# Optimization experiments

Measured on AMD Instinct MI355X. Metric: run time of the kernel, lower is better.

The kernel has to match this reference:

```python
import jax, jax.numpy as jnp
import numpy as np

N_NODES = 10000   # n_entity
VOCAB = 50000     # nvoc
EMBED = 300       # nembed
HID = 256         # nhid
REP = 8           # words per node name


def setup_inputs() -> dict:
    key = jax.random.key(0)
    k0, k1, k2, k3, k4 = jax.random.split(key, 5)
    nodes_rep = jax.random.randint(k0, (N_NODES + 1, REP), 0, VOCAB)
    emb = jax.random.normal(k1, (VOCAB, EMBED), dtype=jnp.float32) * 0.02
    # dense (row-scaled) adjacency, as the module does adj @ support
    adj = jax.random.uniform(k2, (N_NODES, N_NODES), dtype=jnp.float32) / N_NODES
    W1 = jax.random.normal(k3, (EMBED, HID), dtype=jnp.float32) * 0.05
    b1 = jnp.zeros((HID,), dtype=jnp.float32)
    W2 = jax.random.normal(k4, (HID, HID), dtype=jnp.float32) * 0.05
    b2 = jnp.zeros((HID,), dtype=jnp.float32)
    return {"nodes_rep": nodes_rep, "emb": emb, "adj": adj,
            "W1": W1, "b1": b1, "W2": W2, "b2": b2}


def reference(nodes_rep, emb, adj, W1, b1, W2, b2):
    # get_nodes_embed, model == 'gcn_no_dropout'
    x = emb[nodes_rep[1:]]            # [N, REP, EMBED] gather
    x = jnp.max(x, axis=1)            # max-pool over name words -> [N, EMBED]
    # GraphConvolution: adj @ (x @ W) + b
    h = jax.nn.leaky_relu(adj @ (x @ W1) + b1)   # [N, HID]
    h = jax.nn.leaky_relu(adj @ (h @ W2) + b2)   # [N, HID]
    return h
```

## Files before the change

### kernel.cpp

```cpp
#include <hip/hip_runtime.h>
#include <stdint.h>


#define N_NODES 10000
#define MP      10112
#define KP      10048
#define EMB     300
#define EKP     320
#define HID     256
#define SLOPE   0.01f

typedef __attribute__((ext_vector_type(8))) short          bf16x8;
typedef __attribute__((ext_vector_type(4))) float          f32x4;
typedef __attribute__((ext_vector_type(8))) unsigned short ushort8;
typedef __attribute__((ext_vector_type(4))) unsigned short ushort4v;

__device__ __forceinline__ unsigned short f2b(float f) {
    union { float f; unsigned u; } v; v.f = f;
    unsigned r = v.u + 0x7FFFu + ((v.u >> 16) & 1u);
    return (unsigned short)(r >> 16);
}

__device__ __forceinline__ void g2l16(const void* gptr, const void* ldsptr) {
    __builtin_amdgcn_global_load_lds(
        (const __attribute__((address_space(1))) void*)(uintptr_t)gptr,
        (__attribute__((address_space(3))) void*)(uint32_t)(uintptr_t)ldsptr,
        16, 0, 0);
}

__global__ void convert_adj(const float* __restrict__ adj,
                            unsigned short* __restrict__ out) {
    const int r  = blockIdx.y;
    const int c0 = (blockIdx.x * 256 + threadIdx.x) * 8;
    if (c0 >= KP) return;
    ushort8 v = {};
    if (r < N_NODES && c0 + 8 <= N_NODES) {
        const float* src = adj + (size_t)r * N_NODES + c0;
        f32x4 f0 = *(const f32x4*)src;
        f32x4 f1 = *(const f32x4*)(src + 4);
#pragma unroll
        for (int t = 0; t < 4; ++t) { v[t] = f2b(f0[t]); v[t + 4] = f2b(f1[t]); }
    }
    *(ushort8*)(out + (size_t)r * KP + c0) = v;
}

__global__ void gather_max_x(const int* __restrict__ nodes,
                             const float* __restrict__ emb,
                             unsigned short* __restrict__ xb) {
    const int i = blockIdx.x;
    unsigned short* xrow = xb + (size_t)i * EKP;
    if (i >= N_NODES) {
        for (int e = threadIdx.x; e < EKP; e += 256) xrow[e] = 0;
        return;
    }
    const int* idx = nodes + (i + 1) * 8;
    int id[8];
#pragma unroll
    for (int r = 0; r < 8; ++r) id[r] = idx[r];
    for (int e = threadIdx.x; e < EKP; e += 256) {
        unsigned short v = 0;
        if (e < EMB) {
            float m = emb[(size_t)id[0] * EMB + e];
#pragma unroll
            for (int r = 1; r < 8; ++r) m = fmaxf(m, emb[(size_t)id[r] * EMB + e]);
            v = f2b(m);
        }
        xrow[e] = v;
    }
}

__global__ void prep_w(const float* __restrict__ W, unsigned short* __restrict__ Wt,
                       int K, int Kpad) {
    const int o = blockIdx.x * 256 + threadIdx.x;
    if (o >= HID * Kpad) return;
    const int n = o / Kpad, k = o % Kpad;
    Wt[o] = (k < K) ? f2b(W[(size_t)k * HID + n]) : 0;
}

__global__ void transpose_bf16(const unsigned short* __restrict__ in,
                               unsigned short* __restrict__ out) {
    __shared__ unsigned short t[32][33];
    const int kt = blockIdx.x * 32, nt = blockIdx.y * 32;
    const int x = threadIdx.x, y0 = threadIdx.y;
#pragma unroll
    for (int yy = y0; yy < 32; yy += 8)
        t[yy][x] = in[(size_t)(kt + yy) * HID + nt + x];
    __syncthreads();
#pragma unroll
    for (int yy = y0; yy < 32; yy += 8)
        out[(size_t)(nt + yy) * KP + kt + x] = t[x][yy];
}

template <int MODE>
__launch_bounds__(256, 3)
__global__ void gemm_bt(const unsigned short* __restrict__ A, int ldA,
                        const unsigned short* __restrict__ Bt, int ldB,
                        void* __restrict__ Cout, int ldC,
                        int Ktot, int kChunk, size_t partStride) {
    const int tid  = threadIdx.x;
    const int wave = tid >> 6, lane = tid & 63;
    const int wm = wave >> 1, wn = wave & 1;
    const int l16 = lane & 15, quad = lane >> 4;
    const int tileM = blockIdx.x * 128;
    const int tileN = blockIdx.y * 128;
    const int kStart = (MODE == 1) ? (int)blockIdx.z * kChunk : 0;
    const int kLen   = min(kChunk, Ktot - kStart);

    __shared__ unsigned short ldsA[128 * 64];
    __shared__ unsigned short ldsB[128 * 64];

    const unsigned short* Ag = A  + (size_t)(tileM + (tid >> 3)) * ldA + kStart + ((tid & 7) * 8);
    const unsigned short* Bg = Bt + (size_t)(tileN + (tid >> 3)) * ldB + kStart + ((tid & 7) * 8);
    unsigned short* lA = &ldsA[tid * 8];
    unsigned short* lB = &ldsB[tid * 8];
    const size_t aStep = (size_t)32 * ldA;
    const size_t bStep = (size_t)32 * ldB;

    const unsigned short* pa0 = &ldsA[(wm * 64 + l16) * 64 + quad * 8];
    const unsigned short* pb0 = &ldsB[(wn * 64 + l16) * 64 + quad * 8];

    f32x4 acc[4][4] = {};
    const int kIters = kLen >> 6;

    for (int kt = 0; kt < kIters; ++kt) {
        __syncthreads();
#pragma unroll
        for (int i = 0; i < 4; ++i) {
            g2l16(Ag + i * aStep, lA + i * 2048);
            g2l16(Bg + i * bStep, lB + i * 2048);
        }
        Ag += 64; Bg += 64;
        __syncthreads();
#pragma unroll
        for (int kk = 0; kk < 64; kk += 32) {
            bf16x8 af[4], bq[4];
#pragma unroll
            for (int i = 0; i < 4; ++i) af[i] = *(const bf16x8*)(pa0 + i * 1024 + kk);
#pragma unroll
            for (int j = 0; j < 4; ++j) bq[j] = *(const bf16x8*)(pb0 + j * 1024 + kk);
#pragma unroll
            for (int i = 0; i < 4; ++i)
#pragma unroll
                for (int j = 0; j < 4; ++j)
                    acc[i][j] = __builtin_amdgcn_mfma_f32_16x16x32_bf16(
                        af[i], bq[j], acc[i][j], 0, 0, 0);
        }
    }

    if (MODE == 0) {
        unsigned short* C = (unsigned short*)Cout;
#pragma unroll
        for (int i = 0; i < 4; ++i)
#pragma unroll
            for (int r = 0; r < 4; ++r) {
                const int row = tileM + wm * 64 + i * 16 + quad * 4 + r;
#pragma unroll
                for (int j = 0; j < 4; ++j) {
                    const int col = tileN + wn * 64 + j * 16 + l16;
                    C[(size_t)row * ldC + col] = f2b(acc[i][j][r]);
                }
            }
    } else {
        float* C = (float*)Cout + (size_t)blockIdx.z * partStride;
#pragma unroll
        for (int i = 0; i < 4; ++i)
#pragma unroll
            for (int r = 0; r < 4; ++r) {
                const int row = tileM + wm * 64 + i * 16 + quad * 4 + r;
#pragma unroll
                for (int j = 0; j < 4; ++j) {
                    const int col = tileN + wn * 64 + j * 16 + l16;
                    C[(size_t)row * ldC + col] = acc[i][j][r];
                }
            }
    }
}

template <int OUT_BF16>
__global__ void reduce_bias_lrelu(const float* __restrict__ parts, size_t partStride,
                                  const float* __restrict__ bias,
                                  void* __restrict__ out, int outRows) {
    const int idx = blockIdx.x * 256 + threadIdx.x;
    const int e4  = idx * 4;
    const int row = e4 >> 8;
    const int col = e4 & 255;
    if (row >= MP) return;
    f32x4 s = *(const f32x4*)(parts + e4);
#pragma unroll
    for (int p = 1; p < 4; ++p) s += *(const f32x4*)(parts + p * partStride + e4);
    s += *(const f32x4*)(bias + col);
#pragma unroll
    for (int t = 0; t < 4; ++t) s[t] = s[t] > 0.0f ? s[t] : SLOPE * s[t];
    if (OUT_BF16) {
        ushort4v o;
#pragma unroll
        for (int t = 0; t < 4; ++t) o[t] = f2b(s[t]);
        *(ushort4v*)((unsigned short*)out + e4) = o;
    } else if (row < outRows) {
        *(f32x4*)((float*)out + e4) = s;
    }
}

extern "C" void kernel_launch(void* const* d_in, const int* in_sizes, int n_in,
                              void* d_out, int out_size, void* d_ws, size_t ws_size,
                              hipStream_t stream) {
    const int*   nodes = (const int*)d_in[0];
    const float* emb   = (const float*)d_in[1];
    const float* adj   = (const float*)d_in[2];
    const float* W1    = (const float*)d_in[3];
    const float* b1    = (const float*)d_in[4];
    const float* W2    = (const float*)d_in[5];
    const float* b2    = (const float*)d_in[6];

    char* ws = (char*)d_ws;
    size_t o = 0;
    unsigned short* adjb = (unsigned short*)(ws + o); o += (size_t)MP * KP * 2;
    unsigned short* xb   = (unsigned short*)(ws + o); o += (size_t)MP * EKP * 2;
    unsigned short* w1t  = (unsigned short*)(ws + o); o += (size_t)HID * EKP * 2;
    unsigned short* w2t  = (unsigned short*)(ws + o); o += (size_t)HID * HID * 2;
    unsigned short* u1   = (unsigned short*)(ws + o); o += (size_t)MP * HID * 2;
    unsigned short* u1t  = (unsigned short*)(ws + o); o += (size_t)HID * KP * 2;
    unsigned short* h1   = (unsigned short*)(ws + o); o += (size_t)MP * HID * 2;
    unsigned short* u2   = (unsigned short*)(ws + o); o += (size_t)MP * HID * 2;
    unsigned short* u2t  = (unsigned short*)(ws + o); o += (size_t)HID * KP * 2;
    float*          parts= (float*)(ws + o);          o += (size_t)4 * MP * HID * 4;

    const size_t PSTRIDE = (size_t)MP * HID;

    convert_adj <<<dim3(5, MP), 256, 0, stream>>>(adj, adjb);
    gather_max_x<<<MP, 256, 0, stream>>>(nodes, emb, xb);
    prep_w      <<<(HID * EKP + 255) / 256, 256, 0, stream>>>(W1, w1t, EMB, EKP);
    prep_w      <<<(HID * HID + 255) / 256, 256, 0, stream>>>(W2, w2t, HID, HID);

    gemm_bt<0><<<dim3(79, 2, 1), 256, 0, stream>>>(xb, EKP, w1t, EKP, u1, HID,
                                                   EKP, EKP, 0);
    transpose_bf16<<<dim3(KP / 32, HID / 32), dim3(32, 8), 0, stream>>>(u1, u1t);

    gemm_bt<1><<<dim3(79, 2, 4), 256, 0, stream>>>(adjb, KP, u1t, KP, parts, HID,
                                                   KP, 2560, PSTRIDE);
    reduce_bias_lrelu<1><<<(MP * HID / 4 + 255) / 256, 256, 0, stream>>>(
        parts, PSTRIDE, b1, h1, MP);

    gemm_bt<0><<<dim3(79, 2, 1), 256, 0, stream>>>(h1, HID, w2t, HID, u2, HID,
                                                   HID, HID, 0);
    transpose_bf16<<<dim3(KP / 32, HID / 32), dim3(32, 8), 0, stream>>>(u2, u2t);

    gemm_bt<1><<<dim3(79, 2, 4), 256, 0, stream>>>(adjb, KP, u2t, KP, parts, HID,
                                                   KP, 2560, PSTRIDE);
    reduce_bias_lrelu<0><<<(MP * HID / 4 + 255) / 256, 256, 0, stream>>>(
        parts, PSTRIDE, b2, d_out, N_NODES);
}
```

Measured before the change: 808.7 us.

## Fuse fp32-to-bf16 adjacency conversion into adj GEMM with full-width N tile

Removes the separate pass that converted the dense adjacency to a bf16 workspace copy. The new GEMM reads fp32 adj directly, converts it in registers and stores it to LDS, and prefetches the next A tile during compute. Each block covers the full 256-column output, so adj is streamed once per layer. This trades the extra write and read of the bf16 copy for reading twice as many bytes of fp32 per layer, plus conversion work and register pressure inside the GEMM loop.

```diff
diff --git a/kernel.cpp b/kernel.cpp
--- a/kernel.cpp
+++ b/kernel.cpp
@@ -26,22 +26,6 @@
         (const __attribute__((address_space(1))) void*)(uintptr_t)gptr,
         (__attribute__((address_space(3))) void*)(uint32_t)(uintptr_t)ldsptr,
         16, 0, 0);
-}
-
-__global__ void convert_adj(const float* __restrict__ adj,
-                            unsigned short* __restrict__ out) {
-    const int r  = blockIdx.y;
-    const int c0 = (blockIdx.x * 256 + threadIdx.x) * 8;
-    if (c0 >= KP) return;
-    ushort8 v = {};
-    if (r < N_NODES && c0 + 8 <= N_NODES) {
-        const float* src = adj + (size_t)r * N_NODES + c0;
-        f32x4 f0 = *(const f32x4*)src;
-        f32x4 f1 = *(const f32x4*)(src + 4);
-#pragma unroll
-        for (int t = 0; t < 4; ++t) { v[t] = f2b(f0[t]); v[t + 4] = f2b(f1[t]); }
-    }
-    *(ushort8*)(out + (size_t)r * KP + c0) = v;
 }
 
 __global__ void gather_max_x(const int* __restrict__ nodes,
@@ -91,26 +75,22 @@
         out[(size_t)(nt + yy) * KP + kt + x] = t[x][yy];
 }
 
-template <int MODE>
 __launch_bounds__(256, 3)
 __global__ void gemm_bt(const unsigned short* __restrict__ A, int ldA,
                         const unsigned short* __restrict__ Bt, int ldB,
-                        void* __restrict__ Cout, int ldC,
-                        int Ktot, int kChunk, size_t partStride) {
+                        unsigned short* __restrict__ C, int ldC, int Ktot) {
     const int tid  = threadIdx.x;
     const int wave = tid >> 6, lane = tid & 63;
     const int wm = wave >> 1, wn = wave & 1;
     const int l16 = lane & 15, quad = lane >> 4;
     const int tileM = blockIdx.x * 128;
     const int tileN = blockIdx.y * 128;
-    const int kStart = (MODE == 1) ? (int)blockIdx.z * kChunk : 0;
-    const int kLen   = min(kChunk, Ktot - kStart);
 
     __shared__ unsigned short ldsA[128 * 64];
     __shared__ unsigned short ldsB[128 * 64];
 
-    const unsigned short* Ag = A  + (size_t)(tileM + (tid >> 3)) * ldA + kStart + ((tid & 7) * 8);
-    const unsigned short* Bg = Bt + (size_t)(tileN + (tid >> 3)) * ldB + kStart + ((tid & 7) * 8);
+    const unsigned short* Ag = A  + (size_t)(tileM + (tid >> 3)) * ldA + ((tid & 7) * 8);
+    const unsigned short* Bg = Bt + (size_t)(tileN + (tid >> 3)) * ldB + ((tid & 7) * 8);
     unsigned short* lA = &ldsA[tid * 8];
     unsigned short* lB = &ldsB[tid * 8];
     const size_t aStep = (size_t)32 * ldA;
@@ -120,7 +100,7 @@
     const unsigned short* pb0 = &ldsB[(wn * 64 + l16) * 64 + quad * 8];
 
     f32x4 acc[4][4] = {};
-    const int kIters = kLen >> 6;
+    const int kIters = Ktot >> 6;
 
     for (int kt = 0; kt < kIters; ++kt) {
         __syncthreads();
@@ -147,33 +127,118 @@
         }
     }
 
-    if (MODE == 0) {
-        unsigned short* C = (unsigned short*)Cout;
-#pragma unroll
-        for (int i = 0; i < 4; ++i)
-#pragma unroll
-            for (int r = 0; r < 4; ++r) {
-                const int row = tileM + wm * 64 + i * 16 + quad * 4 + r;
-#pragma unroll
-                for (int j = 0; j < 4; ++j) {
-                    const int col = tileN + wn * 64 + j * 16 + l16;
-                    C[(size_t)row * ldC + col] = f2b(acc[i][j][r]);
-                }
+#pragma unroll
+    for (int i = 0; i < 4; ++i)
+#pragma unroll
+        for (int r = 0; r < 4; ++r) {
+            const int row = tileM + wm * 64 + i * 16 + quad * 4 + r;
+#pragma unroll
+            for (int j = 0; j < 4; ++j) {
+                const int col = tileN + wn * 64 + j * 16 + l16;
+                C[(size_t)row * ldC + col] = f2b(acc[i][j][r]);
             }
-    } else {
-        float* C = (float*)Cout + (size_t)blockIdx.z * partStride;
-#pragma unroll
-        for (int i = 0; i < 4; ++i)
-#pragma unroll
-            for (int r = 0; r < 4; ++r) {
-                const int row = tileM + wm * 64 + i * 16 + quad * 4 + r;
-#pragma unroll
-                for (int j = 0; j < 4; ++j) {
-                    const int col = tileN + wn * 64 + j * 16 + l16;
-                    C[(size_t)row * ldC + col] = acc[i][j][r];
-                }
+        }
+}
+
+__launch_bounds__(256, 3)
+__global__ void gemm_adj_f32(const float* __restrict__ A,
+                             const unsigned short* __restrict__ Bt,
+                             float* __restrict__ parts,
+                             int kChunk, size_t partStride) {
+    const int tid  = threadIdx.x;
+    const int wave = tid >> 6, lane = tid & 63;
+    const int l16 = lane & 15, quad = lane >> 4;
+    const int tileM  = blockIdx.x * 64;
+    const int kStart = (int)blockIdx.z * kChunk;
+    const int kLen   = min(kChunk, KP - kStart);
+    const int kIters = kLen >> 6;
+
+    __shared__ unsigned short ldsA[64 * 64];
+    __shared__ unsigned short ldsB[256 * 64];
+
+    const int arow = tid >> 3;
+    const int acol = (tid & 7) * 8;
+
+    const unsigned short* Bg = Bt + (size_t)(tid >> 3) * KP + kStart + acol;
+    unsigned short* lB = &ldsB[tid * 8];
+
+    const unsigned short* pa0 = &ldsA[l16 * 64 + quad * 8];
+    const unsigned short* pb0 = &ldsB[(wave * 64 + l16) * 64 + quad * 8];
+
+    f32x4 acc[4][4] = {};
+
+    f32x4 av[2][2];
+
+    auto loadA = [&](int kt) {
+#pragma unroll
+        for (int r = 0; r < 2; ++r) {
+            const int grow = tileM + arow + r * 32;
+            const int gc   = kStart + kt * 64 + acol;
+            if (grow < N_NODES && gc + 8 <= N_NODES) {
+                const float* src = A + (size_t)grow * N_NODES + gc;
+                av[r][0] = *(const f32x4*)src;
+                av[r][1] = *(const f32x4*)(src + 4);
+            } else if (grow < N_NODES) {
+#pragma unroll
+                for (int h = 0; h < 2; ++h)
+#pragma unroll
+                    for (int t = 0; t < 4; ++t)
+                        av[r][h][t] = (gc + h * 4 + t < N_NODES)
+                                    ? A[(size_t)grow * N_NODES + gc + h * 4 + t] : 0.0f;
+            } else {
+                av[r][0] = (f32x4){0.f, 0.f, 0.f, 0.f};
+                av[r][1] = (f32x4){0.f, 0.f, 0.f, 0.f};
             }
-    }
+        }
+    };
+
+    loadA(0);
+
+    for (int kt = 0; kt < kIters; ++kt) {
+        __syncthreads();
+#pragma unroll
+        for (int r = 0; r < 2; ++r) {
+            ushort8 o;
+#pragma unroll
+            for (int h = 0; h < 2; ++h)
+#pragma unroll
+            for (int t = 0; t < 4; ++t) o[h * 4 + t] = f2b(av[r][h][t]);
+            *(ushort8*)(&ldsA[(arow + r * 32) * 64 + acol]) = o;
+        }
+        const unsigned short* bg = Bg + kt * 64;
+#pragma unroll
+        for (int i = 0; i < 8; ++i)
+            g2l16(bg + (size_t)i * 32 * KP, lB + i * 2048);
+        __syncthreads();
+        if (kt + 1 < kIters) loadA(kt + 1);
+#pragma unroll
+        for (int kk = 0; kk < 64; kk += 32) {
+            bf16x8 af[4], bq[4];
+#pragma unroll
+            for (int i = 0; i < 4; ++i) af[i] = *(const bf16x8*)(pa0 + i * 1024 + kk);
+#pragma unroll
+            for (int j = 0; j < 4; ++j) bq[j] = *(const bf16x8*)(pb0 + j * 1024 + kk);
+#pragma unroll
+            for (int i = 0; i < 4; ++i)
+#pragma unroll
+                for (int j = 0; j < 4; ++j)
+                    acc[i][j] = __builtin_amdgcn_mfma_f32_16x16x32_bf16(
+                        af[i], bq[j], acc[i][j], 0, 0, 0);
+        }
+    }
+
+    float* C = parts + (size_t)blockIdx.z * partStride;
+#pragma unroll
+    for (int i = 0; i < 4; ++i)
+#pragma unroll
+        for (int r = 0; r < 4; ++r) {
+            const int row = tileM + i * 16 + quad * 4 + r;
+#pragma unroll
+            for (int j = 0; j < 4; ++j) {
+                const int col = wave * 64 + j * 16 + l16;
+                C[(size_t)row * HID + col] = acc[i][j][r];
+            }
+        }
 }
 
 template <int OUT_BF16>
@@ -214,7 +279,6 @@
 
     char* ws = (char*)d_ws;
     size_t o = 0;
-    unsigned short* adjb = (unsigned short*)(ws + o); o += (size_t)MP * KP * 2;
     unsigned short* xb   = (unsigned short*)(ws + o); o += (size_t)MP * EKP * 2;
     unsigned short* w1t  = (unsigned short*)(ws + o); o += (size_t)HID * EKP * 2;
     unsigned short* w2t  = (unsigned short*)(ws + o); o += (size_t)HID * HID * 2;
@@ -227,26 +291,21 @@
 
     const size_t PSTRIDE = (size_t)MP * HID;
 
-    convert_adj <<<dim3(5, MP), 256, 0, stream>>>(adj, adjb);
     gather_max_x<<<MP, 256, 0, stream>>>(nodes, emb, xb);
     prep_w      <<<(HID * EKP + 255) / 256, 256, 0, stream>>>(W1, w1t, EMB, EKP);
     prep_w      <<<(HID * HID + 255) / 256, 256, 0, stream>>>(W2, w2t, HID, HID);
 
-    gemm_bt<0><<<dim3(79, 2, 1), 256, 0, stream>>>(xb, EKP, w1t, EKP, u1, HID,
-                                                   EKP, EKP, 0);
+    gemm_bt<<<dim3(79, 2), 256, 0, stream>>>(xb, EKP, w1t, EKP, u1, HID, EKP);
     transpose_bf16<<<dim3(KP / 32, HID / 32), dim3(32, 8), 0, stream>>>(u1, u1t);
 
-    gemm_bt<1><<<dim3(79, 2, 4), 256, 0, stream>>>(adjb, KP, u1t, KP, parts, HID,
-                                                   KP, 2560, PSTRIDE);
+    gemm_adj_f32<<<dim3(158, 1, 4), 256, 0, stream>>>(adj, u1t, parts, 2560, PSTRIDE);
     reduce_bias_lrelu<1><<<(MP * HID / 4 + 255) / 256, 256, 0, stream>>>(
         parts, PSTRIDE, b1, h1, MP);
 
-    gemm_bt<0><<<dim3(79, 2, 1), 256, 0, stream>>>(h1, HID, w2t, HID, u2, HID,
-                                                   HID, HID, 0);
+    gemm_bt<<<dim3(79, 2), 256, 0, stream>>>(h1, HID, w2t, HID, u2, HID, HID);
     transpose_bf16<<<dim3(KP / 32, HID / 32), dim3(32, 8), 0, stream>>>(u2, u2t);
 
-    gemm_bt<1><<<dim3(79, 2, 4), 256, 0, stream>>>(adjb, KP, u2t, KP, parts, HID,
-                                                   KP, 2560, PSTRIDE);
+    gemm_adj_f32<<<dim3(158, 1, 4), 256, 0, stream>>>(adj, u2t, parts, 2560, PSTRIDE);
     reduce_bias_lrelu<0><<<(MP * HID / 4 + 255) / 256, 256, 0, stream>>>(
         parts, PSTRIDE, b2, d_out, N_NODES);
 }
```

Result: no change. 798.6 us (-1.3%).
